# Kernel optimization log

Hardware: AMD Instinct MI355X
Metric: run time of the kernel (lower is better)

## Reference

```python
import jax, jax.numpy as jnp
import numpy as np

BIG_NEG = -1.0e6  # constants.big_negative


def setup_inputs() -> dict:
    key = jax.random.key(0)
    ks = jax.random.split(key, 10)
    B, N, NF, HNF, M, T = 2048, 100, 128, 128, 128, 12
    hidden_output_nodes = jax.random.normal(ks[0], (B, N, HNF), dtype=jnp.float32)
    input_nodes = jax.random.normal(ks[1], (B, N, NF), dtype=jnp.float32)
    node_mask = jax.random.uniform(ks[2], (B, N)) < 0.8
    node_mask = node_mask.at[:, 0].set(True)  # avoid fully-masked rows
    s = 0.05
    W_emb = jax.random.normal(ks[3], (M, NF + HNF), dtype=jnp.float32) * s
    b_emb = jnp.zeros((M,), dtype=jnp.float32)
    W_ih = jax.random.normal(ks[4], (4 * M, M), dtype=jnp.float32) * s
    b_ih = jnp.zeros((4 * M,), dtype=jnp.float32)
    W_hh = jax.random.normal(ks[5], (4 * M, M), dtype=jnp.float32) * s
    b_hh = jnp.zeros((4 * M,), dtype=jnp.float32)
    return {
        "hidden_output_nodes": hidden_output_nodes,
        "input_nodes": input_nodes,
        "W_emb": W_emb, "b_emb": b_emb,
        "W_ih": W_ih, "b_ih": b_ih, "W_hh": W_hh, "b_hh": b_hh,
        "node_mask": node_mask,
        "lstm_computations": T,
    }


def _set2vec(hidden_output_nodes, input_nodes, W_emb, b_emb, W_ih, b_ih, W_hh, b_hh, node_mask, T):
    B = input_nodes.shape[0]
    M = W_emb.shape[0]
    # memory: [B, N, M]
    cat = jnp.concatenate((hidden_output_nodes, input_nodes), axis=2)
    memory = jnp.einsum("bnf,mf->bnm", cat, W_emb) + b_emb
    energy_mask = (~node_mask).astype(memory.dtype) * BIG_NEG  # [B, N]

    zeros = jnp.zeros((B, M), dtype=memory.dtype)

    def step(carry, _):
        lstm_in, h, c = carry
        # LSTMCell (PyTorch gate order: i, f, g, o)
        gates = lstm_in @ W_ih.T + b_ih + h @ W_hh.T + b_hh
        i, f, g, o = jnp.split(gates, 4, axis=-1)
        c = jax.nn.sigmoid(f) * c + jax.nn.sigmoid(i) * jnp.tanh(g)
        q = jax.nn.sigmoid(o) * jnp.tanh(c)  # query / new hidden state
        # dot-product attention read over the node memory
        energies = jnp.einsum("bm,bnm->bn", q, memory) + energy_mask
        attn = jax.nn.softmax(energies, axis=1)
        read = jnp.einsum("bn,bnm->bm", attn, memory)
        return (read, q, c), None

    (read, q, _), _ = jax.lax.scan(step, (zeros, zeros, zeros), None, length=T)
    return jnp.concatenate((q, read), axis=1)  # [B, 2*M]


def reference(hidden_output_nodes, input_nodes, W_emb, b_emb, W_ih, b_ih, W_hh, b_hh, node_mask, lstm_computations):
    return _set2vec(hidden_output_nodes, input_nodes, W_emb, b_emb, W_ih, b_ih, W_hh, b_hh, node_mask, lstm_computations)
```

## Files before the change

### kernel.cpp

```cpp
#include <hip/hip_runtime.h>
#include <hip/hip_fp16.h>
#include <math.h>

#define BIG_NEG  (-1.0e6f)
#define NN   100
#define MD   128
#define KD   256
#define G4   512
#define NB   4
#define MP2  68

#define WS_WGF_H  32768
#define WS_BIAS_F 81920

typedef _Float16 f16x2 __attribute__((ext_vector_type(2)));
typedef _Float16 f16x8 __attribute__((ext_vector_type(8)));
typedef float    f32x4 __attribute__((ext_vector_type(4)));

__device__ __forceinline__ float sigm(float x) { return 1.0f / (1.0f + __expf(-x)); }

extern "C" __global__ void prep_kernel(const float* __restrict__ W_emb,
                                       const float* __restrict__ W_ih,
                                       const float* __restrict__ b_ih,
                                       const float* __restrict__ W_hh,
                                       const float* __restrict__ b_hh,
                                       float* __restrict__ ws) {
    int tid = blockIdx.x * blockDim.x + threadIdx.x;
    int nth = gridDim.x * blockDim.x;
    __half* WF    = (__half*)ws;
    __half* WG    = (__half*)ws + WS_WGF_H;
    float*  biasc = ws + WS_BIAS_F;
    for (int i = tid; i < 32768; i += nth) {
        int kg = i >> 10, m = (i >> 3) & 127, j = i & 7;
        WF[i] = __float2half(W_emb[m * 256 + kg * 8 + j]);
    }
    for (int i = tid; i < 131072; i += nth) {
        int kc = i >> 12, g = (i >> 3) & 511, j = i & 7;
        int k = kc * 8 + j;
        float w = (k < 128) ? W_ih[g * 128 + k] : W_hh[g * 128 + (k - 128)];
        WG[i] = __float2half(w);
    }
    for (int i = tid; i < 512; i += nth) biasc[i] = b_ih[i] + b_hh[i];
}

extern "C" __global__ __launch_bounds__(1024, 4)
void set2vec_main(const float* __restrict__ hidden,
                  const float* __restrict__ input,
                  const float* __restrict__ b_emb,
                  const unsigned char* __restrict__ mask_bytes,
                  const int* __restrict__ Tptr,
                  const float* __restrict__ ws,
                  float* __restrict__ out) {
    __shared__ __half2 mem2[NB][NN][MP2];
    __shared__ __half  xcath[NB][KD];
    __shared__ float   xcat2[NB][KD];
    __shared__ float   cbuf[NB][MD];
    __shared__ float   emask[NB][NN];
    __shared__ float   bbuf[G4];
    __shared__ int     mask_is_u8;
    __shared__ float   gbuf[NB][G4];
    __shared__ float   epart[NB][2][NN];
    __shared__ float   abuf[NB][NN];

    const int tid  = threadIdx.x;
    const int b0   = blockIdx.x * NB;
    const int lane = tid & 63, wv = tid >> 6;
    const int ln15 = lane & 15, lhi = lane >> 4;
    const __half* WF = (const __half*)ws;

    if (tid == 0) {
        int nz = 0;
        for (int i = 0; i < 64; ++i)
            if ((i & 3) && mask_bytes[i]) nz = 1;
        mask_is_u8 = nz;
    }

    {
        const float be0 = b_emb[0 * 16 + ln15], be1 = b_emb[1 * 16 + ln15];
        const float be2 = b_emb[2 * 16 + ln15], be3 = b_emb[3 * 16 + ln15];
        const float be4 = b_emb[4 * 16 + ln15], be5 = b_emb[5 * 16 + ln15];
        const float be6 = b_emb[6 * 16 + ln15], be7 = b_emb[7 * 16 + ln15];
        __half* memh = (__half*)mem2;
        for (int tile = wv; tile < 25; tile += 16) {
            f32x4 acc0 = {be0, be0, be0, be0}, acc1 = {be1, be1, be1, be1};
            f32x4 acc2 = {be2, be2, be2, be2}, acc3 = {be3, be3, be3, be3};
            f32x4 acc4 = {be4, be4, be4, be4}, acc5 = {be5, be5, be5, be5};
            f32x4 acc6 = {be6, be6, be6, be6}, acc7 = {be7, be7, be7, be7};

            const int rA     = tile * 16 + ln15;
            const int rAok   = rA < NB * NN;
            const long gbase = ((long)(b0 * NN + rA)) << 7;

            #pragma unroll 1
            for (int mk = 0; mk < 8; ++mk) {
                f16x8 aF;
                if (rAok) {
                    int k0 = mk * 32 + lhi * 8;
                    const float* src = (k0 < 128) ? (hidden + gbase + k0)
                                                  : (input + gbase + (k0 - 128));
                    float4 v0 = *(const float4*)src;
                    float4 v1 = *(const float4*)(src + 4);
                    union { f16x8 v; f16x2 h[4]; } au;
                    au.h[0] = __builtin_bit_cast(f16x2, __builtin_amdgcn_cvt_pkrtz(v0.x, v0.y));
                    au.h[1] = __builtin_bit_cast(f16x2, __builtin_amdgcn_cvt_pkrtz(v0.z, v0.w));
                    au.h[2] = __builtin_bit_cast(f16x2, __builtin_amdgcn_cvt_pkrtz(v1.x, v1.y));
                    au.h[3] = __builtin_bit_cast(f16x2, __builtin_amdgcn_cvt_pkrtz(v1.z, v1.w));
                    aF = au.v;
                } else {
                    aF = (f16x8)(_Float16)0.0f;
                }
                const __half* wrow = WF + ((mk * 4 + lhi) * 128 + ln15) * 8;
#define EMB_CT(CT, ACC) { \
                union { uint4 u; f16x8 v; } bu; \
                bu.u = *(const uint4*)(wrow + (CT * 16) * 8); \
                ACC = __builtin_amdgcn_mfma_f32_16x16x32_f16(aF, bu.v, ACC, 0, 0, 0); }
                EMB_CT(0, acc0) EMB_CT(1, acc1) EMB_CT(2, acc2) EMB_CT(3, acc3)
                EMB_CT(4, acc4) EMB_CT(5, acc5) EMB_CT(6, acc6) EMB_CT(7, acc7)
#undef EMB_CT
            }
#define EMB_WR(CT, ACC) { \
            _Pragma("unroll") \
            for (int reg = 0; reg < 4; ++reg) { \
                int r = tile * 16 + lhi * 4 + reg; \
                if (r < NB * NN) { \
                    int bb = r / NN, n = r - (r / NN) * NN; \
                    memh[(bb * NN + n) * (2 * MP2) + CT * 16 + ln15] = __float2half(ACC[reg]); \
                } } }
            EMB_WR(0, acc0) EMB_WR(1, acc1) EMB_WR(2, acc2) EMB_WR(3, acc3)
            EMB_WR(4, acc4) EMB_WR(5, acc5) EMB_WR(6, acc6) EMB_WR(7, acc7)
#undef EMB_WR
        }
    }

    ((float*)xcat2)[tid] = 0.0f;
    ((__half*)xcath)[tid] = __float2half(0.0f);
    if (tid < NB * MD) ((float*)cbuf)[tid] = 0.0f;
    if (tid < G4) bbuf[tid] = ws[WS_BIAS_F + tid];
    if (tid < NB * NN) {
        int bb = tid / NN, n = tid - bb * NN;
        long mrow = (long)(b0 + bb) * NN + n;
        int valid = mask_is_u8 ? (mask_bytes[mrow] != 0)
                               : (((const int*)mask_bytes)[mrow] != 0);
        emask[bb][n] = valid ? 0.0f : BIG_NEG;
    }
    __syncthreads();

    const int T = Tptr[0];

    const uint4* WgB = (const uint4*)((const __half*)ws + WS_WGF_H);
    const int ct0 = wv * 2, ct1 = wv * 2 + 1;
    const __half* aBase = &xcath[ln15 & 3][lhi * 8];

    const int e_act = tid < 800;
    const int e_bb  = tid / 200;
    const int e_r   = tid - e_bb * 200;
    const int e_mh  = e_r / 100;
    const int e_n   = e_r - e_mh * 100;

    for (int step = 0; step < T; ++step) {
        {
            f32x4 ga = {0.f, 0.f, 0.f, 0.f}, gb = {0.f, 0.f, 0.f, 0.f};
            #pragma unroll 2
            for (int ks = 0; ks < 8; ++ks) {
                union { uint4 u; f16x8 v; } a, bA, bB;
                a.u = *(const uint4*)(aBase + ks * 32);
                int kc = ks * 4 + lhi;
                bA.u = WgB[kc * 512 + ct0 * 16 + ln15];
                ga = __builtin_amdgcn_mfma_f32_16x16x32_f16(a.v, bA.v, ga, 0, 0, 0);
                bB.u = WgB[kc * 512 + ct1 * 16 + ln15];
                gb = __builtin_amdgcn_mfma_f32_16x16x32_f16(a.v, bB.v, gb, 0, 0, 0);
            }
            if (lhi == 0) {
                #pragma unroll
                for (int r = 0; r < 4; ++r) {
                    gbuf[r][ct0 * 16 + ln15] = ga[r];
                    gbuf[r][ct1 * 16 + ln15] = gb[r];
                }
            }
        }
        __syncthreads();
        if (tid < NB * MD) {
            int bb = tid >> 7, m = tid & 127;
            float gi = gbuf[bb][m]       + bbuf[m];
            float gf = gbuf[bb][128 + m] + bbuf[128 + m];
            float gg = gbuf[bb][256 + m] + bbuf[256 + m];
            float go = gbuf[bb][384 + m] + bbuf[384 + m];
            float c  = cbuf[bb][m];
            c = sigm(gf) * c + sigm(gi) * tanhf(gg);
            float qv = sigm(go) * tanhf(c);
            cbuf[bb][m] = c;
            xcat2[bb][128 + m] = qv;
            xcath[bb][128 + m] = __float2half(qv);
        }
        __syncthreads();
        if (e_act) {
            const uint4*  mr4 = (const uint4*)&mem2[e_bb][e_n][e_mh * 32];
            const float4* qv4 = (const float4*)&xcat2[e_bb][128 + e_mh * 64];
            float e = 0.0f;
            #pragma unroll
            for (int i = 0; i < 8; ++i) {
                uint4  mu = mr4[i];
                float4 qa = qv4[2 * i], qb = qv4[2 * i + 1];
                float2 m0 = __half22float2(*(__half2*)&mu.x);
                float2 m1 = __half22float2(*(__half2*)&mu.y);
                float2 m2 = __half22float2(*(__half2*)&mu.z);
                float2 m3 = __half22float2(*(__half2*)&mu.w);
                e = fmaf(qa.x, m0.x, e); e = fmaf(qa.y, m0.y, e);
                e = fmaf(qa.z, m1.x, e); e = fmaf(qa.w, m1.y, e);
                e = fmaf(qb.x, m2.x, e); e = fmaf(qb.y, m2.y, e);
                e = fmaf(qb.z, m3.x, e); e = fmaf(qb.w, m3.y, e);
            }
            ((float*)epart)[tid] = e;
        }
        __syncthreads();
        if (tid < 256) {
            int bb = tid >> 6, l = tid & 63;
            const float* ep = &epart[bb][0][0];
            float e0 = ep[l] + ep[100 + l] + emask[bb][l];
            float e1 = -INFINITY;
            if (l < 36) {
                int n1 = l + 64;
                e1 = ep[n1] + ep[100 + n1] + emask[bb][n1];
            }
            float mx = fmaxf(e0, e1);
            for (int off = 32; off; off >>= 1) mx = fmaxf(mx, __shfl_xor(mx, off, 64));
            float p0 = __expf(e0 - mx);
            float p1 = (l < 36) ? __expf(e1 - mx) : 0.0f;
            float s = p0 + p1;
            for (int off = 32; off; off >>= 1) s += __shfl_xor(s, off, 64);
            float inv = 1.0f / s;
            abuf[bb][l] = p0 * inv;
            if (l < 36) abuf[bb][l + 64] = p1 * inv;
        }
        __syncthreads();
        if (tid < 256) {
            int bb = tid >> 6, mp = tid & 63;
            const float*   ar  = abuf[bb];
            const __half2* mrp = &mem2[bb][0][mp];
            float r0 = 0, r1 = 0, r2 = 0, r3 = 0, s0 = 0, s1 = 0, s2 = 0, s3 = 0;
            #pragma unroll 5
            for (int n = 0; n < 100; n += 4) {
                float4  av = *(const float4*)(ar + n);
                __half2 h0 = mrp[n * MP2],       h1 = mrp[(n + 1) * MP2];
                __half2 h2 = mrp[(n + 2) * MP2], h3 = mrp[(n + 3) * MP2];
                float2 f0 = __half22float2(h0), f1 = __half22float2(h1);
                float2 f2 = __half22float2(h2), f3 = __half22float2(h3);
                r0 = fmaf(av.x, f0.x, r0); s0 = fmaf(av.x, f0.y, s0);
                r1 = fmaf(av.y, f1.x, r1); s1 = fmaf(av.y, f1.y, s1);
                r2 = fmaf(av.z, f2.x, r2); s2 = fmaf(av.z, f2.y, s2);
                r3 = fmaf(av.w, f3.x, r3); s3 = fmaf(av.w, f3.y, s3);
            }
            float rx = (r0 + r1) + (r2 + r3);
            float ry = (s0 + s1) + (s2 + s3);
            int m = mp * 2;
            xcat2[bb][m]     = rx;
            xcat2[bb][m + 1] = ry;
            xcath[bb][m]     = __float2half(rx);
            xcath[bb][m + 1] = __float2half(ry);
        }
        __syncthreads();
    }

    {
        int bb = tid >> 8, j = tid & 255;
        float v = (j < 128) ? xcat2[bb][128 + j] : xcat2[bb][j - 128];
        out[((long)(b0 + bb) << 8) + j] = v;
    }
}

extern "C" void kernel_launch(void* const* d_in, const int* in_sizes, int n_in,
                              void* d_out, int out_size, void* d_ws, size_t ws_size,
                              hipStream_t stream) {
    const float* hidden = (const float*)d_in[0];
    const float* input  = (const float*)d_in[1];
    const float* W_emb  = (const float*)d_in[2];
    const float* b_emb  = (const float*)d_in[3];
    const float* W_ih   = (const float*)d_in[4];
    const float* b_ih   = (const float*)d_in[5];
    const float* W_hh   = (const float*)d_in[6];
    const float* b_hh   = (const float*)d_in[7];
    const unsigned char* mask = (const unsigned char*)d_in[8];
    const int*  Tptr    = (const int*)d_in[9];
    float* ws   = (float*)d_ws;
    float* outp = (float*)d_out;

    hipLaunchKernelGGL(prep_kernel, dim3(128), dim3(256), 0, stream,
                       W_emb, W_ih, b_ih, W_hh, b_hh, ws);
    hipLaunchKernelGGL(set2vec_main, dim3(512), dim3(1024), 0, stream,
                       hidden, input, b_emb, mask, Tptr, ws, outp);
}
```

Measured before the change: 201.1 us.

## Hoist LSTM gate weights into registers and pad shared buffers to cut bank conflicts

Measured after the change: 185.1 us. 1.09x faster.

```diff
diff --git a/kernel.cpp b/kernel.cpp
--- a/kernel.cpp
+++ b/kernel.cpp
@@ -9,6 +9,7 @@
 #define G4   512
 #define NB   4
 #define MP2  68
+#define XPAD 288
 
 #define WS_WGF_H  32768
 #define WS_BIAS_F 81920
@@ -52,14 +53,14 @@
                   const float* __restrict__ ws,
                   float* __restrict__ out) {
     __shared__ __half2 mem2[NB][NN][MP2];
-    __shared__ __half  xcath[NB][KD];
+    __shared__ __half  xcath[NB][XPAD];
     __shared__ float   xcat2[NB][KD];
     __shared__ float   cbuf[NB][MD];
     __shared__ float   emask[NB][NN];
     __shared__ float   bbuf[G4];
     __shared__ int     mask_is_u8;
     __shared__ float   gbuf[NB][G4];
-    __shared__ float   epart[NB][2][NN];
+    __shared__ float   epart[NB][NN][2];
     __shared__ float   abuf[NB][NN];
 
     const int tid  = threadIdx.x;
@@ -132,8 +133,16 @@
         }
     }
 
+    const uint4* WgB = (const uint4*)((const __half*)ws + WS_WGF_H);
+    const int ct0 = wv * 2, ct1 = wv * 2 + 1;
+#define LDW(KS) \
+    const uint4 wA##KS = WgB[((KS) * 4 + lhi) * 512 + ct0 * 16 + ln15]; \
+    const uint4 wB##KS = WgB[((KS) * 4 + lhi) * 512 + ct1 * 16 + ln15];
+    LDW(0) LDW(1) LDW(2) LDW(3) LDW(4) LDW(5) LDW(6) LDW(7)
+#undef LDW
+
+    for (int i = tid; i < NB * XPAD; i += 1024) ((__half*)xcath)[i] = __float2half(0.0f);
     ((float*)xcat2)[tid] = 0.0f;
-    ((__half*)xcath)[tid] = __float2half(0.0f);
     if (tid < NB * MD) ((float*)cbuf)[tid] = 0.0f;
     if (tid < G4) bbuf[tid] = ws[WS_BIAS_F + tid];
     if (tid < NB * NN) {
@@ -147,29 +156,25 @@
 
     const int T = Tptr[0];
 
-    const uint4* WgB = (const uint4*)((const __half*)ws + WS_WGF_H);
-    const int ct0 = wv * 2, ct1 = wv * 2 + 1;
     const __half* aBase = &xcath[ln15 & 3][lhi * 8];
 
     const int e_act = tid < 800;
     const int e_bb  = tid / 200;
     const int e_r   = tid - e_bb * 200;
-    const int e_mh  = e_r / 100;
-    const int e_n   = e_r - e_mh * 100;
+    const int e_n   = e_r >> 1;
+    const int e_mh  = e_r & 1;
 
     for (int step = 0; step < T; ++step) {
         {
             f32x4 ga = {0.f, 0.f, 0.f, 0.f}, gb = {0.f, 0.f, 0.f, 0.f};
-            #pragma unroll 2
-            for (int ks = 0; ks < 8; ++ks) {
-                union { uint4 u; f16x8 v; } a, bA, bB;
-                a.u = *(const uint4*)(aBase + ks * 32);
-                int kc = ks * 4 + lhi;
-                bA.u = WgB[kc * 512 + ct0 * 16 + ln15];
-                ga = __builtin_amdgcn_mfma_f32_16x16x32_f16(a.v, bA.v, ga, 0, 0, 0);
-                bB.u = WgB[kc * 512 + ct1 * 16 + ln15];
-                gb = __builtin_amdgcn_mfma_f32_16x16x32_f16(a.v, bB.v, gb, 0, 0, 0);
-            }
+#define GS(KS) { \
+            union { uint4 u; f16x8 v; } a, ba, bc; \
+            a.u  = *(const uint4*)(aBase + (KS) * 32); \
+            ba.u = wA##KS; bc.u = wB##KS; \
+            ga = __builtin_amdgcn_mfma_f32_16x16x32_f16(a.v, ba.v, ga, 0, 0, 0); \
+            gb = __builtin_amdgcn_mfma_f32_16x16x32_f16(a.v, bc.v, gb, 0, 0, 0); }
+            GS(0) GS(1) GS(2) GS(3) GS(4) GS(5) GS(6) GS(7)
+#undef GS
             if (lhi == 0) {
                 #pragma unroll
                 for (int r = 0; r < 4; ++r) {
@@ -210,17 +215,16 @@
                 e = fmaf(qb.x, m2.x, e); e = fmaf(qb.y, m2.y, e);
                 e = fmaf(qb.z, m3.x, e); e = fmaf(qb.w, m3.y, e);
             }
-            ((float*)epart)[tid] = e;
+            epart[e_bb][e_n][e_mh] = e;
         }
         __syncthreads();
         if (tid < 256) {
             int bb = tid >> 6, l = tid & 63;
-            const float* ep = &epart[bb][0][0];
-            float e0 = ep[l] + ep[100 + l] + emask[bb][l];
+            float e0 = epart[bb][l][0] + epart[bb][l][1] + emask[bb][l];
             float e1 = -INFINITY;
             if (l < 36) {
                 int n1 = l + 64;
-                e1 = ep[n1] + ep[100 + n1] + emask[bb][n1];
+                e1 = epart[bb][n1][0] + epart[bb][n1][1] + emask[bb][n1];
             }
             float mx = fmaxf(e0, e1);
             for (int off = 32; off; off >>= 1) mx = fmaxf(mx, __shfl_xor(mx, off, 64));
```
